# Kernel tuning notes

Measured on AMD Instinct MI355X. Metric: run time of the kernel, lower is better.

Reference implementation:

```python
import jax, jax.numpy as jnp
import numpy as np

B=4; TEXT_LEN=64; IMG=256; P=16; DIM=1024; HEADS=16; LAYERS=2; MLP=4; VOCAB=50000; TDIM=256; MAXTXT=2048
HP=IMG//P; NPATCH=HP*HP; HD=DIM//HEADS; EPS=1e-5

def _ln(x, g, b):
    m = jnp.mean(x, -1, keepdims=True)
    v = jnp.mean((x - m) ** 2, -1, keepdims=True)
    return (x - m) / jnp.sqrt(v + EPS) * g + b

def _rope_cos_sin(n, d):
    inv = 1.0 / (10000.0 ** (jnp.arange(0, d, 2, dtype=jnp.float32) / d))
    f = jnp.outer(jnp.arange(n, dtype=jnp.float32), inv)
    e = jnp.concatenate([f, f], -1)  # [n, d]
    return jnp.cos(e), jnp.sin(e)

def _rot_half(x):
    # matches torch: cat((-x[...,1::2], x[...,::2]), -1)
    return jnp.concatenate([-x[..., 1::2], x[..., ::2]], -1)

def _forward(noisy_images, text_tokens, timesteps, W_tok, pos_text, W_patch, pos_img, cls_tok,
             W_t1, b_t1, W_t2, b_t2, ln1_g, ln1_b, Wq, Wk, Wv, Wo, ln2_g, ln2_b,
             Wm1, Wm2, Wada, b_ada, fn_g, fn_b, W_final, b_final):
    Bn = noisy_images.shape[0]
    # text embed: one_hot @ W_tok.T == gather of columns of W_tok [DIM, VOCAB]
    text_emb = jnp.transpose(jnp.take(W_tok, text_tokens, axis=1), (1, 2, 0)) + pos_text[:, :TEXT_LEN]
    # image patches: [B,3,HP,P,HP,P] -> [B,HP,WP,C,P,P] -> [B,NPATCH, 3*P*P]
    patches = noisy_images.reshape(Bn, 3, HP, P, HP, P).transpose(0, 2, 4, 1, 3, 5).reshape(Bn, NPATCH, 3 * P * P)
    img_emb = patches @ W_patch.T + pos_img
    img_emb = jnp.concatenate([jnp.broadcast_to(cls_tok, (Bn, 1, DIM)), img_emb], 1)
    x = jnp.concatenate([text_emb, img_emb], 1)  # [B, N, DIM]
    N = x.shape[1]
    # sinusoidal timestep embedding (dim=256)
    half = TDIM // 2
    freqs = jnp.exp(-jnp.log(10000.0) * jnp.arange(half, dtype=jnp.float32) / half)
    args = timesteps.astype(jnp.float32)[:, None] * freqs[None]
    temb_raw = jnp.concatenate([jnp.cos(args), jnp.sin(args)], -1)
    t_emb = jax.nn.silu(temb_raw @ W_t1.T + b_t1) @ W_t2.T + b_t2  # [B, DIM]
    cos, sin = _rope_cos_sin(N, HD)
    scale = HD ** -0.5
    for l in range(LAYERS):
        mod = jax.nn.silu(t_emb) @ Wada[l].T + b_ada[l]
        sh_msa, sc_msa, g_msa, sh_mlp, sc_mlp, g_mlp = jnp.split(mod, 6, -1)
        xn = _ln(x, ln1_g[l], ln1_b[l]) * (1 + sc_msa[:, None]) + sh_msa[:, None]
        q = (xn @ Wq[l].T).reshape(Bn, N, HEADS, HD).transpose(0, 2, 1, 3)
        k = (xn @ Wk[l].T).reshape(Bn, N, HEADS, HD).transpose(0, 2, 1, 3)
        v = (xn @ Wv[l].T).reshape(Bn, N, HEADS, HD).transpose(0, 2, 1, 3)
        q = q * cos + _rot_half(q) * sin
        k = k * cos + _rot_half(k) * sin
        att = jax.nn.softmax(jnp.einsum('bhnd,bhmd->bhnm', q, k) * scale, -1)
        o = jnp.einsum('bhnm,bhmd->bhnd', att, v).transpose(0, 2, 1, 3).reshape(Bn, N, DIM)
        x = x + g_msa[:, None] * (o @ Wo[l].T)
        xn2 = _ln(x, ln2_g[l], ln2_b[l]) * (1 + sc_mlp[:, None]) + sh_mlp[:, None]
        mlp = jax.nn.gelu(xn2 @ Wm1[l].T, approximate=False) @ Wm2[l].T
        x = x + g_mlp[:, None] * mlp
    img_tok = x[:, TEXT_LEN + 1:]
    out = _ln(img_tok, fn_g, fn_b) @ W_final.T + b_final  # [B, NPATCH, 3*P*P]
    out = out.reshape(Bn, HP, HP, 3, P, P).transpose(0, 3, 1, 4, 2, 5).reshape(Bn, 3, IMG, IMG)
    return out

def setup_inputs() -> dict:
    key = jax.random.key(0)
    ks = jax.random.split(key, 24)
    def n(k, shape, s=0.02):
        return (jax.random.normal(k, shape, jnp.float32) * s).astype(jnp.float32)
    inp = {}
    inp['noisy_images'] = jax.random.normal(ks[0], (B, 3, IMG, IMG), jnp.float32)
    inp['text_tokens'] = jax.random.randint(ks[1], (B, TEXT_LEN), 0, VOCAB)
    inp['timesteps'] = jax.random.randint(ks[2], (B,), 0, 1000)
    inp['W_tok'] = n(ks[3], (DIM, VOCAB))
    inp['pos_text'] = n(ks[4], (1, MAXTXT, DIM))
    inp['W_patch'] = n(ks[5], (DIM, 3 * P * P))
    inp['pos_img'] = n(ks[6], (1, NPATCH, DIM))
    inp['cls_tok'] = n(ks[7], (1, 1, DIM))
    inp['W_t1'] = n(ks[8], (DIM, TDIM)); inp['b_t1'] = jnp.zeros((DIM,), jnp.float32)
    inp['W_t2'] = n(ks[9], (DIM, DIM)); inp['b_t2'] = jnp.zeros((DIM,), jnp.float32)
    inp['ln1_g'] = jnp.ones((LAYERS, DIM), jnp.float32); inp['ln1_b'] = jnp.zeros((LAYERS, DIM), jnp.float32)
    inp['Wq'] = n(ks[10], (LAYERS, DIM, DIM))
    inp['Wk'] = n(ks[11], (LAYERS, DIM, DIM))
    inp['Wv'] = n(ks[12], (LAYERS, DIM, DIM))
    inp['Wo'] = n(ks[13], (LAYERS, DIM, DIM))
    inp['ln2_g'] = jnp.ones((LAYERS, DIM), jnp.float32); inp['ln2_b'] = jnp.zeros((LAYERS, DIM), jnp.float32)
    inp['Wm1'] = n(ks[14], (LAYERS, MLP * DIM, DIM))
    inp['Wm2'] = n(ks[15], (LAYERS, DIM, MLP * DIM))
    inp['Wada'] = n(ks[16], (LAYERS, 6 * DIM, DIM)); inp['b_ada'] = jnp.zeros((LAYERS, 6 * DIM), jnp.float32)
    inp['fn_g'] = jnp.ones((DIM,), jnp.float32); inp['fn_b'] = jnp.zeros((DIM,), jnp.float32)
    inp['W_final'] = n(ks[17], (3 * P * P, DIM)); inp['b_final'] = jnp.zeros((3 * P * P,), jnp.float32)
    return inp

def reference(noisy_images, text_tokens, timesteps, W_tok, pos_text, W_patch, pos_img, cls_tok,
              W_t1, b_t1, W_t2, b_t2, ln1_g, ln1_b, Wq, Wk, Wv, Wo, ln2_g, ln2_b,
              Wm1, Wm2, Wada, b_ada, fn_g, fn_b, W_final, b_final):
    return _forward(noisy_images, text_tokens, timesteps, W_tok, pos_text, W_patch, pos_img, cls_tok,
                    W_t1, b_t1, W_t2, b_t2, ln1_g, ln1_b, Wq, Wk, Wv, Wo, ln2_g, ln2_b,
                    Wm1, Wm2, Wada, b_ada, fn_g, fn_b, W_final, b_final)
```

## Files before the change

### kernel.cpp

```cpp
#include <hip/hip_runtime.h>
#include <math.h>

constexpr int kBn    = 4;
constexpr int kText  = 64;
constexpr int kImg   = 256;
constexpr int kDim   = 1024;
constexpr int kHeads = 16;
constexpr int kHd    = 64;
constexpr int kNp    = 256;
constexpr int kTok   = 321;
constexpr int kVocab = 50000;
constexpr int kTdim  = 256;
constexpr int kMlp   = 4096;
constexpr int kScLd  = 328;
constexpr float kEps = 1e-5f;

typedef __attribute__((ext_vector_type(8))) short short8;
typedef __attribute__((ext_vector_type(4))) float f32x4;

__device__ __forceinline__ short f2bf(float x) {
  unsigned u = __builtin_bit_cast(unsigned, x);
  unsigned r = (u + 0x7FFFu + ((u >> 16) & 1u)) >> 16;
  return (short)r;
}

struct GemmM {
  const short* A; const short* B; float* C; const float* E;
  int M, N, K, lda, ldb, ldc;
  long sA0, sA1, sB0, sB1, sC0, sC1;
  int innerB, ldE, rowsPB;
  float alpha;
  int nSplit, splitLen;
  long partStride;
};

template<int EPI, bool PART, bool OUTBF>
__global__ __launch_bounds__(256) void gemm_mfma(GemmM p) {
  int bz = blockIdx.z;
  int split = 0;
  if (PART) { split = bz % p.nSplit; bz /= p.nSplit; }
  int b1 = bz % p.innerB, b0 = bz / p.innerB;
  const short* A = p.A + b0*p.sA0 + b1*p.sA1;
  const short* B = p.B + b0*p.sB0 + b1*p.sB1;
  long cbase = b0*p.sC0 + b1*p.sC1 + (PART ? (long)split * p.partStride : 0);
  const float* E = p.E;

  int kBeg = PART ? split * p.splitLen : 0;
  int kEnd = PART ? min(p.K, kBeg + p.splitLen) : p.K;

  __shared__ short As[64*72];
  __shared__ short Bs[64*72];

  int tid  = threadIdx.x;
  int lane = tid & 63, widx = tid >> 6;
  int quad = lane >> 4, ln = lane & 15;
  int wm = (widx >> 1) * 32, wn = (widx & 1) * 32;
  int n0 = blockIdx.x * 64, m0 = blockIdx.y * 64;

  f32x4 zero = {0.f, 0.f, 0.f, 0.f};
  f32x4 acc[2][2];
  acc[0][0] = zero; acc[0][1] = zero; acc[1][0] = zero; acc[1][1] = zero;

  short8 ra[2], rb[2];
  auto issueLoads = [&](int k0) {
#pragma unroll
    for (int r = 0; r < 2; ++r) {
      int c = tid + 256*r;
      int row = c >> 3, kc = c & 7;
      int gk = k0 + kc*8;
      {
        int gm = m0 + row;
        const short* src = A + (long)gm * p.lda + gk;
        if (gm < p.M && gk + 8 <= kEnd) {
          ra[r] = *(const short8*)src;
        } else {
          short8 t = {0,0,0,0,0,0,0,0};
          if (gm < p.M) {
#pragma unroll
            for (int j = 0; j < 8; ++j) if (gk + j < kEnd) t[j] = src[j];
          }
          ra[r] = t;
        }
      }
      {
        int gn = n0 + row;
        const short* src = B + (long)gn * p.ldb + gk;
        if (gn < p.N && gk + 8 <= kEnd) {
          rb[r] = *(const short8*)src;
        } else {
          short8 t = {0,0,0,0,0,0,0,0};
          if (gn < p.N) {
#pragma unroll
            for (int j = 0; j < 8; ++j) if (gk + j < kEnd) t[j] = src[j];
          }
          rb[r] = t;
        }
      }
    }
  };

  issueLoads(kBeg);
  for (int k0 = kBeg; k0 < kEnd; k0 += 64) {
#pragma unroll
    for (int r = 0; r < 2; ++r) {
      int c = tid + 256*r;
      int row = c >> 3, kc = c & 7;
      *(short8*)&As[row*72 + kc*8] = ra[r];
      *(short8*)&Bs[row*72 + kc*8] = rb[r];
    }
    __syncthreads();
    if (k0 + 64 < kEnd) issueLoads(k0 + 64);
#pragma unroll
    for (int ks = 0; ks < 2; ++ks) {
      short8 a0 = *(const short8*)&As[(wm +      ln)*72 + ks*32 + quad*8];
      short8 a1 = *(const short8*)&As[(wm + 16 + ln)*72 + ks*32 + quad*8];
      short8 b0 = *(const short8*)&Bs[(wn +      ln)*72 + ks*32 + quad*8];
      short8 b1 = *(const short8*)&Bs[(wn + 16 + ln)*72 + ks*32 + quad*8];
      acc[0][0] = __builtin_amdgcn_mfma_f32_16x16x32_bf16(a0, b0, acc[0][0], 0, 0, 0);
      acc[0][1] = __builtin_amdgcn_mfma_f32_16x16x32_bf16(a0, b1, acc[0][1], 0, 0, 0);
      acc[1][0] = __builtin_amdgcn_mfma_f32_16x16x32_bf16(a1, b0, acc[1][0], 0, 0, 0);
      acc[1][1] = __builtin_amdgcn_mfma_f32_16x16x32_bf16(a1, b1, acc[1][1], 0, 0, 0);
    }
    __syncthreads();
  }

#pragma unroll
  for (int mi = 0; mi < 2; ++mi)
#pragma unroll
    for (int ni = 0; ni < 2; ++ni)
#pragma unroll
      for (int reg = 0; reg < 4; ++reg) {
        int gm = m0 + wm + mi*16 + quad*4 + reg;
        int gn = n0 + wn + ni*16 + ln;
        if (gm >= p.M || gn >= p.N) continue;
        long co = cbase + (long)gm * p.ldc + gn;
        float v = acc[mi][ni][reg] * p.alpha;
        if (!PART) {
          if (EPI == 1) v += E[gn];
          else if (EPI == 3) v = 0.5f*v*(1.f + erff(v*0.70710678118654752f));
          else if (EPI == 4) v += E[(long)gm*p.ldE + gn];
          else if (EPI == 5) v = p.C[co] + E[(long)(gm / p.rowsPB)*p.ldE + gn] * v;
        }
        if (OUTBF) ((short*)p.C)[co] = f2bf(v);
        else       p.C[co] = v;
      }
}

static GemmM mkm(const short* A, const short* B, float* C,
                 int M, int N, int K, int lda, int ldb, int ldc) {
  GemmM p; p.A = A; p.B = B; p.C = C; p.E = nullptr;
  p.M = M; p.N = N; p.K = K; p.lda = lda; p.ldb = ldb; p.ldc = ldc;
  p.sA0 = p.sA1 = p.sB0 = p.sB1 = p.sC0 = p.sC1 = 0;
  p.innerB = 1; p.ldE = 0; p.rowsPB = 1; p.alpha = 1.f;
  p.nSplit = 1; p.splitLen = 0; p.partStride = 0;
  return p;
}

static void run_gemm(hipStream_t s, int epi, bool outbf, const GemmM& p, int nb) {
  dim3 g((p.N + 63)/64, (p.M + 63)/64, nb), b(256, 1, 1);
  if (outbf) {
    if (epi == 3) gemm_mfma<3,false,true><<<g,b,0,s>>>(p);
    else          gemm_mfma<0,false,true><<<g,b,0,s>>>(p);
    return;
  }
  switch (epi) {
    case 0: gemm_mfma<0,false,false><<<g,b,0,s>>>(p); break;
    case 1: gemm_mfma<1,false,false><<<g,b,0,s>>>(p); break;
    case 4: gemm_mfma<4,false,false><<<g,b,0,s>>>(p); break;
    case 5: gemm_mfma<5,false,false><<<g,b,0,s>>>(p); break;
  }
}

static void run_gemm_part(hipStream_t s, const GemmM& p, int nb) {
  dim3 g((p.N + 63)/64, (p.M + 63)/64, nb * p.nSplit), b(256, 1, 1);
  gemm_mfma<0,true,false><<<g,b,0,s>>>(p);
}

template<int EPI>
__global__ __launch_bounds__(256) void reduce_split(
    const float* __restrict__ part, long partStride, int S,
    float* __restrict__ C, const float* __restrict__ E,
    int Mv, int Nv, int ldc, long sC0, long sC1, int innerB,
    int ldE, int rowsPB, int total) {
  int idx = blockIdx.x*256 + threadIdx.x;
  if (idx >= total) return;
  int n = idx % Nv;
  int m = (idx / Nv) % Mv;
  int bz = idx / (Nv * Mv);
  int b1 = bz % innerB, b0 = bz / innerB;
  long co = b0*sC0 + b1*sC1 + (long)m*ldc + n;
  float v = 0.f;
  for (int s = 0; s < S; ++s) v += part[(long)s*partStride + co];
  if (EPI == 1) v += E[n];
  else if (EPI == 3) v = 0.5f*v*(1.f + erff(v*0.70710678118654752f));
  else if (EPI == 4) v += E[(long)m*ldE + n];
  else if (EPI == 5) v = C[co] + E[(long)(m / rowsPB)*ldE + n] * v;
  C[co] = v;
}

static void run_reduce(hipStream_t st, int epi, const float* part, long pStride, int S,
                       float* C, const float* E, int Mv, int Nv, int ldc,
                       long sC0, long sC1, int innerB, int nbTot, int ldE, int rowsPB) {
  int total = nbTot * Mv * Nv;
  dim3 g((total + 255)/256), b(256);
  switch (epi) {
    case 0: reduce_split<0><<<g,b,0,st>>>(part,pStride,S,C,E,Mv,Nv,ldc,sC0,sC1,innerB,ldE,rowsPB,total); break;
    case 1: reduce_split<1><<<g,b,0,st>>>(part,pStride,S,C,E,Mv,Nv,ldc,sC0,sC1,innerB,ldE,rowsPB,total); break;
    case 3: reduce_split<3><<<g,b,0,st>>>(part,pStride,S,C,E,Mv,Nv,ldc,sC0,sC1,innerB,ldE,rowsPB,total); break;
    case 4: reduce_split<4><<<g,b,0,st>>>(part,pStride,S,C,E,Mv,Nv,ldc,sC0,sC1,innerB,ldE,rowsPB,total); break;
    case 5: reduce_split<5><<<g,b,0,st>>>(part,pStride,S,C,E,Mv,Nv,ldc,sC0,sC1,innerB,ldE,rowsPB,total); break;
  }
}

__global__ __launch_bounds__(256) void cvt_bf16(const float* __restrict__ src,
                                                short* __restrict__ dst, int n8) {
  int i = blockIdx.x*256 + threadIdx.x;
  if (i >= n8) return;
  float4 a = ((const float4*)src)[2*i];
  float4 b = ((const float4*)src)[2*i + 1];
  short8 o;
  o[0]=f2bf(a.x); o[1]=f2bf(a.y); o[2]=f2bf(a.z); o[3]=f2bf(a.w);
  o[4]=f2bf(b.x); o[5]=f2bf(b.y); o[6]=f2bf(b.z); o[7]=f2bf(b.w);
  *(short8*)(dst + 8L*i) = o;
}

static void cvt(hipStream_t s, const float* src, short* dst, long n) {
  long n8 = n / 8;
  cvt_bf16<<<dim3((unsigned)((n8 + 255)/256)), dim3(256), 0, s>>>(src, dst, (int)n8);
}

template<int EPI>
__global__ __launch_bounds__(256) void gemv4(const float* __restrict__ A,
                                             const float* __restrict__ B,
                                             float* __restrict__ C,
                                             const float* __restrict__ bias,
                                             int N, int K, int ldc) {
  int wave = threadIdx.x >> 6, lane = threadIdx.x & 63;
  int n = blockIdx.x * 4 + wave;
  if (n >= N) return;
  const float* Brow = B + (long)n * K;
  float acc0 = 0.f, acc1 = 0.f, acc2 = 0.f, acc3 = 0.f;
  for (int k = lane * 4; k < K; k += 256) {
    float4 b = *(const float4*)(Brow + k);
    float4 a0 = *(const float4*)(A + 0*K + k);
    float4 a1 = *(const float4*)(A + 1*K + k);
    float4 a2 = *(const float4*)(A + 2*K + k);
    float4 a3 = *(const float4*)(A + 3*K + k);
    acc0 += a0.x*b.x + a0.y*b.y + a0.z*b.z + a0.w*b.w;
    acc1 += a1.x*b.x + a1.y*b.y + a1.z*b.z + a1.w*b.w;
    acc2 += a2.x*b.x + a2.y*b.y + a2.z*b.z + a2.w*b.w;
    acc3 += a3.x*b.x + a3.y*b.y + a3.z*b.z + a3.w*b.w;
  }
#pragma unroll
  for (int off = 32; off; off >>= 1) {
    acc0 += __shfl_xor(acc0, off);
    acc1 += __shfl_xor(acc1, off);
    acc2 += __shfl_xor(acc2, off);
    acc3 += __shfl_xor(acc3, off);
  }
  if (lane == 0) {
    float bs = bias[n];
    float v[4] = {acc0 + bs, acc1 + bs, acc2 + bs, acc3 + bs};
#pragma unroll
    for (int m = 0; m < 4; ++m) {
      float x = v[m];
      if (EPI == 2) x = x / (1.f + expf(-x));
      C[(long)m * ldc + n] = x;
    }
  }
}

__global__ void embed_text_cls(const float* __restrict__ Wtok, const int* __restrict__ toks,
                               const float* __restrict__ pos_text, const float* __restrict__ cls_tok,
                               float* __restrict__ x) {
  int idx = blockIdx.x*256 + threadIdx.x;
  int d = idx % kDim;
  int t = (idx / kDim) % (kText + 1);
  int b = idx / (kDim * (kText + 1));
  float v;
  if (t < kText) {
    int tok = toks[b*kText + t];
    v = Wtok[(long)d*kVocab + tok] + pos_text[(long)t*kDim + d];
  } else {
    v = cls_tok[d];
  }
  x[((long)b*kTok + t)*kDim + d] = v;
}

__global__ void extract_patches(const float* __restrict__ img, short* __restrict__ pat) {
  int idx = blockIdx.x*256 + threadIdx.x;
  int k = idx % 768;
  int p = (idx/768) % kNp;
  int b = idx/(768*kNp);
  int c = k >> 8, py = (k >> 4) & 15, px = k & 15;
  int hp = p >> 4, wp = p & 15;
  pat[idx] = f2bf(img[(((long)(b*3 + c))*kImg + hp*16 + py)*kImg + wp*16 + px]);
}

__global__ void time_freqs(const int* __restrict__ ts, float* __restrict__ temb) {
  int b = blockIdx.x, i = threadIdx.x;
  float f = expf(-9.210340371976184f * (float)i / 128.f);
  float a = (float)ts[b] * f;
  temb[b*kTdim + i] = cosf(a);
  temb[b*kTdim + 128 + i] = sinf(a);
}

__global__ void silu_kernel(const float* __restrict__ in, float* __restrict__ outp, int n) {
  int i = blockIdx.x*256 + threadIdx.x;
  if (i < n) { float x = in[i]; outp[i] = x / (1.f + expf(-x)); }
}

__device__ __forceinline__ float block_sum(float v) {
  __shared__ float sh[4];
  for (int off = 32; off; off >>= 1) v += __shfl_down(v, off);
  if ((threadIdx.x & 63) == 0) sh[threadIdx.x >> 6] = v;
  __syncthreads();
  float s = sh[0] + sh[1] + sh[2] + sh[3];
  __syncthreads();
  return s;
}

__global__ __launch_bounds__(256) void ln_mod_kernel(
    const float* __restrict__ x, const float* __restrict__ g, const float* __restrict__ be,
    const float* __restrict__ mod, int shOff, int scOff, short* __restrict__ outp) {
  int row = blockIdx.x;
  int b = row / kTok;
  const float* xr = x + (long)row*kDim;
  float s = 0.f, s2 = 0.f;
  for (int i = threadIdx.x; i < kDim; i += 256) { float v = xr[i]; s += v; s2 += v*v; }
  s = block_sum(s); s2 = block_sum(s2);
  float m = s / kDim;
  float inv = rsqrtf(s2 / kDim - m*m + kEps);
  const float* mb = mod + (long)b*(6*kDim);
  for (int i = threadIdx.x; i < kDim; i += 256) {
    float xn = (xr[i] - m)*inv*g[i] + be[i];
    outp[(long)row*kDim + i] = f2bf(xn*(1.f + mb[scOff + i]) + mb[shOff + i]);
  }
}

__global__ __launch_bounds__(256) void final_ln_kernel(
    const float* __restrict__ x, const float* __restrict__ g, const float* __restrict__ be,
    short* __restrict__ yn) {
  int row = blockIdx.x;
  int b = row / kNp, p = row % kNp;
  const float* xr = x + ((long)(b*kTok + kText + 1 + p))*kDim;
  float s = 0.f, s2 = 0.f;
  for (int i = threadIdx.x; i < kDim; i += 256) { float v = xr[i]; s += v; s2 += v*v; }
  s = block_sum(s); s2 = block_sum(s2);
  float m = s / kDim;
  float inv = rsqrtf(s2 / kDim - m*m + kEps);
  for (int i = threadIdx.x; i < kDim; i += 256)
    yn[(long)row*kDim + i] = f2bf((xr[i] - m)*inv*g[i] + be[i]);
}

__global__ __launch_bounds__(256) void rope_bf16(const float* __restrict__ qkv,
                                                 short* __restrict__ qb,
                                                 short* __restrict__ kb) {
  int idx = blockIdx.x*256 + threadIdx.x;
  int d = idx & (kDim - 1);
  int r = idx >> 10;
  int n = r % kTok;
  int hd = d & 63;
  int j = hd & 31;
  float inv = expf(-9.210340371976184f * (float)j / 32.f);
  float ang = (float)n * inv;
  float c = cosf(ang), s = sinf(ang);
  const float* row = qkv + (long)r * (3*kDim);
  int base = d - hd;
  float qv = row[d], kv = row[kDim + d];
  float qr, kr;
  if (hd < 32) { qr = -row[base + 2*hd + 1];      kr = -row[kDim + base + 2*hd + 1]; }
  else         { qr =  row[base + 2*(hd - 32)];   kr =  row[kDim + base + 2*(hd - 32)]; }
  qb[idx] = f2bf(qv*c + qr*s);
  kb[idx] = f2bf(kv*c + kr*s);
}

__global__ __launch_bounds__(256) void vtrans_kernel(const float* __restrict__ qkv,
                                                     short* __restrict__ vtb) {
  int idx = blockIdx.x*256 + threadIdx.x;
  int tok = idx % kScLd;
  int hd  = (idx / kScLd) % kHd;
  int h   = (idx / (kScLd*kHd)) % kHeads;
  int b   = idx / (kScLd*kHd*kHeads);
  float v = 0.f;
  if (tok < kTok) v = qkv[((long)(b*kTok + tok))*(3*kDim) + 2*kDim + h*kHd + hd];
  vtb[idx] = f2bf(v);
}

__global__ void softmax_rows(float* __restrict__ sc, short* __restrict__ dst,
                             int rowLen, int rowStride) {
  long row = blockIdx.x;
  float* r = sc + row*rowStride;
  short* d = dst + row*rowStride;
  int t = threadIdx.x;
  float mx = -1e30f;
  for (int i = t; i < rowLen; i += 64) mx = fmaxf(mx, r[i]);
  for (int off = 32; off; off >>= 1) mx = fmaxf(mx, __shfl_xor(mx, off));
  float sum = 0.f;
  for (int i = t; i < rowLen; i += 64) { float e = expf(r[i] - mx); r[i] = e; sum += e; }
  for (int off = 32; off; off >>= 1) sum += __shfl_xor(sum, off);
  float invs = 1.f / sum;
  for (int i = t; i < rowLen; i += 64) d[i] = f2bf(r[i] * invs);
}

__global__ void unpatchify(const float* __restrict__ op, float* __restrict__ outp) {
  int idx = blockIdx.x*256 + threadIdx.x;
  int w = idx & 255;
  int h = (idx >> 8) & 255;
  int c = (idx >> 16) % 3;
  int b = idx / (3 * kImg * kImg);
  int hp = h >> 4, py = h & 15, wp = w >> 4, px = w & 15;
  outp[idx] = op[((long)(b*kNp + hp*16 + wp))*768 + c*256 + py*16 + px];
}

extern "C" void kernel_launch(void* const* d_in, const int* in_sizes, int n_in,
                              void* d_out, int out_size, void* d_ws, size_t ws_size,
                              hipStream_t stream) {
  (void)in_sizes; (void)n_in; (void)out_size;
  const float* noisy    = (const float*)d_in[0];
  const int*   toks     = (const int*)d_in[1];
  const int*   tsteps   = (const int*)d_in[2];
  const float* W_tok    = (const float*)d_in[3];
  const float* pos_text = (const float*)d_in[4];
  const float* W_patch  = (const float*)d_in[5];
  const float* pos_img  = (const float*)d_in[6];
  const float* cls_tok  = (const float*)d_in[7];
  const float* W_t1     = (const float*)d_in[8];
  const float* b_t1     = (const float*)d_in[9];
  const float* W_t2     = (const float*)d_in[10];
  const float* b_t2     = (const float*)d_in[11];
  const float* ln1_g    = (const float*)d_in[12];
  const float* ln1_b    = (const float*)d_in[13];
  const float* Wq       = (const float*)d_in[14];
  const float* Wk       = (const float*)d_in[15];
  const float* Wv       = (const float*)d_in[16];
  const float* Wo       = (const float*)d_in[17];
  const float* ln2_g    = (const float*)d_in[18];
  const float* ln2_b    = (const float*)d_in[19];
  const float* Wm1      = (const float*)d_in[20];
  const float* Wm2      = (const float*)d_in[21];
  const float* Wada     = (const float*)d_in[22];
  const float* b_ada    = (const float*)d_in[23];
  const float* fn_g     = (const float*)d_in[24];
  const float* fn_b     = (const float*)d_in[25];
  const float* W_final  = (const float*)d_in[26];
  const float* b_final  = (const float*)d_in[27];
  float* out = (float*)d_out;

  float* ws = (float*)d_ws;
  auto alloc = [&](long nf) { float* r = ws; ws += nf; return r; };

  const long seqSz = (long)kBn * kTok * kDim;
  float* x    = alloc(seqSz);
  float* qkv  = alloc((long)kBn*kTok*3*kDim);
  float* sc   = alloc((long)kBn*kHeads*kTok*kScLd);
  short* xnb  = (short*)alloc(seqSz/2);
  short* qb   = (short*)alloc(seqSz/2);
  short* kb   = (short*)alloc(seqSz/2);
  short* ob   = (short*)alloc(seqSz/2);
  short* vtb  = (short*)alloc((long)kBn*kHeads*kHd*kScLd/2);
  short* scb  = (short*)alloc((long)kBn*kHeads*kTok*kScLd/2);
  short* patb = (short*)alloc((long)kBn*kNp*768/2);
  short* ynb  = (short*)alloc((long)kBn*kNp*kDim/2);
  short* wbuf = (short*)alloc((long)kMlp*kDim/2);
  float* temb = alloc(kBn*kTdim);
  float* t1   = alloc(kBn*kDim);
  float* temb2= alloc(kBn*kDim);
  float* st   = alloc(kBn*kDim);
  float* mod  = alloc(2L*kBn*6*kDim);
  short* hb   = (short*)sc;
  float* outp = qkv;

  const long scrStride = seqSz;
  float* scr = alloc(4*scrStride);
  bool split_ok = ((char*)ws - (char*)d_ws) <= (long)ws_size;

  embed_text_cls<<<(kBn*(kText+1)*kDim)/256, 256, 0, stream>>>(W_tok, toks, pos_text, cls_tok, x);
  extract_patches<<<(kBn*kNp*768)/256, 256, 0, stream>>>(noisy, patb);
  cvt(stream, W_patch, wbuf, (long)kDim*768);
  {
    GemmM p = mkm(patb, wbuf, split_ok ? scr : (x + (kText+1)*kDim),
                  kNp, kDim, 768, 768, 768, kDim);
    p.sA0 = (long)kNp*768; p.sC0 = (long)kTok*kDim;
    if (split_ok) {
      p.nSplit = 3; p.splitLen = 256; p.partStride = scrStride;
      run_gemm_part(stream, p, kBn);
      run_reduce(stream, 4, scr, scrStride, 3, x + (kText+1)*kDim, pos_img,
                 kNp, kDim, kDim, (long)kTok*kDim, 0, 1, kBn, kDim, 1);
    } else {
      p.E = pos_img; p.ldE = kDim;
      run_gemm(stream, 4, false, p, kBn);
    }
  }
  time_freqs<<<kBn, 128, 0, stream>>>(tsteps, temb);
  gemv4<2><<<kDim/4, 256, 0, stream>>>(temb, W_t1, t1, b_t1, kDim, kTdim, kDim);
  gemv4<1><<<kDim/4, 256, 0, stream>>>(t1, W_t2, temb2, b_t2, kDim, kDim, kDim);
  silu_kernel<<<(kBn*kDim + 255)/256, 256, 0, stream>>>(temb2, st, kBn*kDim);

  for (int l = 0; l < 2; ++l) {
    const float* Wq_l  = Wq  + (long)l*kDim*kDim;
    const float* Wk_l  = Wk  + (long)l*kDim*kDim;
    const float* Wv_l  = Wv  + (long)l*kDim*kDim;
    const float* Wo_l  = Wo  + (long)l*kDim*kDim;
    const float* Wm1_l = Wm1 + (long)l*kMlp*kDim;
    const float* Wm2_l = Wm2 + (long)l*kDim*kMlp;
    float* mod_l = mod + (long)l*kBn*6*kDim;

    gemv4<1><<<(6*kDim)/4, 256, 0, stream>>>(st, Wada + (long)l*6*kDim*kDim, mod_l,
                                             b_ada + (long)l*6*kDim, 6*kDim, kDim, 6*kDim);

    ln_mod_kernel<<<kBn*kTok, 256, 0, stream>>>(x, ln1_g + l*kDim, ln1_b + l*kDim,
                                                mod_l, 0, kDim, xnb);
    cvt(stream, Wq_l, wbuf,                   (long)kDim*kDim);
    cvt(stream, Wk_l, wbuf +   (long)kDim*kDim, (long)kDim*kDim);
    cvt(stream, Wv_l, wbuf + 2L*(long)kDim*kDim, (long)kDim*kDim);
    {
      GemmM p = mkm(xnb, wbuf, qkv, kBn*kTok, 3*kDim, kDim, kDim, kDim, 3*kDim);
      run_gemm(stream, 0, false, p, 1);
    }
    rope_bf16<<<(int)(seqSz/256), 256, 0, stream>>>(qkv, qb, kb);
    vtrans_kernel<<<(kBn*kHeads*kHd*kScLd)/256, 256, 0, stream>>>(qkv, vtb);

    {
      GemmM p = mkm(qb, kb, sc, kTok, kTok, kHd, kDim, kDim, kScLd);
      p.sA0 = (long)kTok*kDim; p.sA1 = kHd;
      p.sB0 = (long)kTok*kDim; p.sB1 = kHd;
      p.sC0 = (long)kHeads*kTok*kScLd; p.sC1 = (long)kTok*kScLd;
      p.innerB = kHeads; p.alpha = 0.125f;
      run_gemm(stream, 0, false, p, kBn*kHeads);
    }
    softmax_rows<<<kBn*kHeads*kTok, 64, 0, stream>>>(sc, scb, kTok, kScLd);
    {
      GemmM p = mkm(scb, vtb, (float*)ob, kTok, kHd, kTok, kScLd, kScLd, kDim);
      p.sA0 = (long)kHeads*kTok*kScLd; p.sA1 = (long)kTok*kScLd;
      p.sB0 = (long)kHeads*kHd*kScLd;  p.sB1 = (long)kHd*kScLd;
      p.sC0 = (long)kTok*kDim;         p.sC1 = kHd;
      p.innerB = kHeads;
      run_gemm(stream, 0, true, p, kBn*kHeads);
    }
    cvt(stream, Wo_l, wbuf, (long)kDim*kDim);
    {
      GemmM p = mkm(ob, wbuf, split_ok ? scr : x, kBn*kTok, kDim, kDim, kDim, kDim, kDim);
      if (split_ok) {
        p.nSplit = 4; p.splitLen = 256; p.partStride = scrStride;
        run_gemm_part(stream, p, 1);
        run_reduce(stream, 5, scr, scrStride, 4, x, mod_l + 2*kDim,
                   kBn*kTok, kDim, kDim, 0, 0, 1, 1, 6*kDim, kTok);
      } else {
        p.E = mod_l + 2*kDim; p.ldE = 6*kDim; p.rowsPB = kTok;
        run_gemm(stream, 5, false, p, 1);
      }
    }
    ln_mod_kernel<<<kBn*kTok, 256, 0, stream>>>(x, ln2_g + l*kDim, ln2_b + l*kDim,
                                                mod_l, 3*kDim, 4*kDim, xnb);
    cvt(stream, Wm1_l, wbuf, (long)kMlp*kDim);
    {
      GemmM p = mkm(xnb, wbuf, (float*)hb, kBn*kTok, kMlp, kDim, kDim, kDim, kMlp);
      run_gemm(stream, 3, true, p, 1);
    }
    cvt(stream, Wm2_l, wbuf, (long)kMlp*kDim);
    {
      GemmM p = mkm(hb, wbuf, split_ok ? scr : x, kBn*kTok, kDim, kMlp, kMlp, kMlp, kDim);
      if (split_ok) {
        p.nSplit = 4; p.splitLen = 1024; p.partStride = scrStride;
        run_gemm_part(stream, p, 1);
        run_reduce(stream, 5, scr, scrStride, 4, x, mod_l + 5*kDim,
                   kBn*kTok, kDim, kDim, 0, 0, 1, 1, 6*kDim, kTok);
      } else {
        p.E = mod_l + 5*kDim; p.ldE = 6*kDim; p.rowsPB = kTok;
        run_gemm(stream, 5, false, p, 1);
      }
    }
  }

  final_ln_kernel<<<kBn*kNp, 256, 0, stream>>>(x, fn_g, fn_b, ynb);
  cvt(stream, W_final, wbuf, (long)768*kDim);
  {
    GemmM p = mkm(ynb, wbuf, split_ok ? scr : outp, kBn*kNp, 768, kDim, kDim, kDim, 768);
    if (split_ok) {
      p.nSplit = 4; p.splitLen = 256; p.partStride = (long)kBn*kNp*768;
      run_gemm_part(stream, p, 1);
      run_reduce(stream, 1, scr, (long)kBn*kNp*768, 4, outp, b_final,
                 kBn*kNp, 768, 768, 0, 0, 1, 1, 0, 1);
    } else {
      p.E = b_final;
      run_gemm(stream, 1, false, p, 1);
    }
  }
  unpatchify<<<(kBn*3*kImg*kImg)/256, 256, 0, stream>>>(outp, out);
}
```

Measured before the change: 823.2 us.

## Add direct-to-LDS double-buffered GEMM, pre-convert weights, fuse reductions with LayerNorm

Adds a new GEMM kernel that loads A/B tiles straight into XOR-swizzled, double-buffered LDS with global_load_lds. It replaces the register-staged padded-LDS path for every GEMM except P·V. All bf16 weight conversions are batched into a few launches at the start, and both adaLN gemvs are hoisted ahead of the layer loop. Split-K reductions are fused into the following residual+LayerNorm kernels and into unpatchify, and softmax now processes four rows per block. The new GEMM has no M/K bounds checks, so partial tiles read rows past M, which risks out-of-range reads on non-multiple-of-64 shapes.

New measurement: 790.5 us. 1.04x faster.

```diff
diff --git a/kernel.cpp b/kernel.cpp
--- a/kernel.cpp
+++ b/kernel.cpp
@@ -24,6 +24,12 @@
   return (short)r;
 }
 
+__device__ __forceinline__ void glds16(const short* g, short* l) {
+  __builtin_amdgcn_global_load_lds(
+      (const __attribute__((address_space(1))) unsigned int*)g,
+      (__attribute__((address_space(3))) unsigned int*)l, 16, 0, 0);
+}
+
 struct GemmM {
   const short* A; const short* B; float* C; const float* E;
   int M, N, K, lda, ldb, ldc;
@@ -34,8 +40,17 @@
   long partStride;
 };
 
+__device__ __forceinline__ float epi_apply(int EPI, const GemmM& p, const float* E,
+                                           long co, int gm, int gn, float v) {
+  if (EPI == 1) v += E[gn];
+  else if (EPI == 3) v = 0.5f*v*(1.f + erff(v*0.70710678118654752f));
+  else if (EPI == 4) v += E[(long)gm*p.ldE + gn];
+  else if (EPI == 5) v = p.C[co] + E[(long)(gm / p.rowsPB)*p.ldE + gn] * v;
+  return v;
+}
+
 template<int EPI, bool PART, bool OUTBF>
-__global__ __launch_bounds__(256) void gemm_mfma(GemmM p) {
+__global__ __launch_bounds__(256) void gemm_gl(GemmM p) {
   int bz = blockIdx.z;
   int split = 0;
   if (PART) { split = bz % p.nSplit; bz /= p.nSplit; }
@@ -48,6 +63,89 @@
   int kBeg = PART ? split * p.splitLen : 0;
   int kEnd = PART ? min(p.K, kBeg + p.splitLen) : p.K;
 
+  __shared__ short As[2][64*64];
+  __shared__ short Bs[2][64*64];
+
+  int tid  = threadIdx.x;
+  int lane = tid & 63, widx = tid >> 6;
+  int quad = lane >> 4, ln = lane & 15;
+  int wm = (widx >> 1) * 32, wn = (widx & 1) * 32;
+  int n0 = blockIdx.x * 64, m0 = blockIdx.y * 64;
+
+  int l3 = lane >> 3, l7 = lane & 7;
+  int kofs = (l7 ^ l3) * 8;
+  const short* gA0 = A + (long)(m0 + 16*widx + l3) * p.lda + kofs;
+  const short* gA1 = gA0 + (long)8 * p.lda;
+  const short* gB0 = B + (long)(n0 + 16*widx + l3) * p.ldb + kofs;
+  const short* gB1 = gB0 + (long)8 * p.ldb;
+  short* lA0 = &As[0][(2*widx)*512];
+  short* lA1 = &As[0][(2*widx+1)*512];
+  short* lB0 = &Bs[0][(2*widx)*512];
+  short* lB1 = &Bs[0][(2*widx+1)*512];
+
+  auto stage = [&](int buf, int k0) {
+    int bo = buf * 4096;
+    glds16(gA0 + k0, lA0 + bo);
+    glds16(gA1 + k0, lA1 + bo);
+    glds16(gB0 + k0, lB0 + bo);
+    glds16(gB1 + k0, lB1 + bo);
+  };
+
+  f32x4 zero = {0.f, 0.f, 0.f, 0.f};
+  f32x4 acc[2][2];
+  acc[0][0] = zero; acc[0][1] = zero; acc[1][0] = zero; acc[1][1] = zero;
+
+  stage(0, kBeg);
+  int buf = 0;
+  for (int k0 = kBeg; k0 < kEnd; k0 += 64) {
+    if (k0 + 64 < kEnd) stage(buf ^ 1, k0 + 64);
+    __syncthreads();
+    const char* Ab = (const char*)&As[buf][0];
+    const char* Bb = (const char*)&Bs[buf][0];
+#pragma unroll
+    for (int ks = 0; ks < 2; ++ks) {
+      int cb = ks*64 + quad*16;
+      int r0 = wm + ln, r1 = wm + 16 + ln, r2 = wn + ln, r3 = wn + 16 + ln;
+      short8 a0 = *(const short8*)(Ab + r0*128 + (cb ^ ((r0 & 7) << 4)));
+      short8 a1 = *(const short8*)(Ab + r1*128 + (cb ^ ((r1 & 7) << 4)));
+      short8 b0 = *(const short8*)(Bb + r2*128 + (cb ^ ((r2 & 7) << 4)));
+      short8 b1 = *(const short8*)(Bb + r3*128 + (cb ^ ((r3 & 7) << 4)));
+      acc[0][0] = __builtin_amdgcn_mfma_f32_16x16x32_bf16(a0, b0, acc[0][0], 0, 0, 0);
+      acc[0][1] = __builtin_amdgcn_mfma_f32_16x16x32_bf16(a0, b1, acc[0][1], 0, 0, 0);
+      acc[1][0] = __builtin_amdgcn_mfma_f32_16x16x32_bf16(a1, b0, acc[1][0], 0, 0, 0);
+      acc[1][1] = __builtin_amdgcn_mfma_f32_16x16x32_bf16(a1, b1, acc[1][1], 0, 0, 0);
+    }
+    __syncthreads();
+    buf ^= 1;
+  }
+
+#pragma unroll
+  for (int mi = 0; mi < 2; ++mi)
+#pragma unroll
+    for (int ni = 0; ni < 2; ++ni)
+#pragma unroll
+      for (int reg = 0; reg < 4; ++reg) {
+        int gm = m0 + wm + mi*16 + quad*4 + reg;
+        int gn = n0 + wn + ni*16 + ln;
+        if (gm >= p.M || gn >= p.N) continue;
+        long co = cbase + (long)gm * p.ldc + gn;
+        float v = acc[mi][ni][reg] * p.alpha;
+        if (!PART) v = epi_apply(EPI, p, E, co, gm, gn, v);
+        if (OUTBF) ((short*)p.C)[co] = f2bf(v);
+        else       p.C[co] = v;
+      }
+}
+
+template<int EPI, bool OUTBF>
+__global__ __launch_bounds__(256) void gemm_mfma(GemmM p) {
+  int bz = blockIdx.z;
+  int b1 = bz % p.innerB, b0 = bz / p.innerB;
+  const short* A = p.A + b0*p.sA0 + b1*p.sA1;
+  const short* B = p.B + b0*p.sB0 + b1*p.sB1;
+  long cbase = b0*p.sC0 + b1*p.sC1;
+  const float* E = p.E;
+  int kEnd = p.K;
+
   __shared__ short As[64*72];
   __shared__ short Bs[64*72];
 
@@ -71,9 +169,8 @@
       {
         int gm = m0 + row;
         const short* src = A + (long)gm * p.lda + gk;
-        if (gm < p.M && gk + 8 <= kEnd) {
-          ra[r] = *(const short8*)src;
-        } else {
+        if (gm < p.M && gk + 8 <= kEnd) ra[r] = *(const short8*)src;
+        else {
           short8 t = {0,0,0,0,0,0,0,0};
           if (gm < p.M) {
 #pragma unroll
@@ -85,9 +182,8 @@
       {
         int gn = n0 + row;
         const short* src = B + (long)gn * p.ldb + gk;
-        if (gn < p.N && gk + 8 <= kEnd) {
-          rb[r] = *(const short8*)src;
-        } else {
+        if (gn < p.N && gk + 8 <= kEnd) rb[r] = *(const short8*)src;
+        else {
           short8 t = {0,0,0,0,0,0,0,0};
           if (gn < p.N) {
 #pragma unroll
@@ -99,8 +195,8 @@
     }
   };
 
-  issueLoads(kBeg);
-  for (int k0 = kBeg; k0 < kEnd; k0 += 64) {
+  issueLoads(0);
+  for (int k0 = 0; k0 < kEnd; k0 += 64) {
 #pragma unroll
     for (int r = 0; r < 2; ++r) {
       int c = tid + 256*r;
@@ -135,12 +231,7 @@
         if (gm >= p.M || gn >= p.N) continue;
         long co = cbase + (long)gm * p.ldc + gn;
         float v = acc[mi][ni][reg] * p.alpha;
-        if (!PART) {
-          if (EPI == 1) v += E[gn];
-          else if (EPI == 3) v = 0.5f*v*(1.f + erff(v*0.70710678118654752f));
-          else if (EPI == 4) v += E[(long)gm*p.ldE + gn];
-          else if (EPI == 5) v = p.C[co] + E[(long)(gm / p.rowsPB)*p.ldE + gn] * v;
-        }
+        v = epi_apply(EPI, p, E, co, gm, gn, v);
         if (OUTBF) ((short*)p.C)[co] = f2bf(v);
         else       p.C[co] = v;
       }
@@ -156,77 +247,68 @@
   return p;
 }
 
-static void run_gemm(hipStream_t s, int epi, bool outbf, const GemmM& p, int nb) {
+static void run_gl(hipStream_t s, int epi, bool outbf, const GemmM& p, int nb) {
   dim3 g((p.N + 63)/64, (p.M + 63)/64, nb), b(256, 1, 1);
   if (outbf) {
-    if (epi == 3) gemm_mfma<3,false,true><<<g,b,0,s>>>(p);
-    else          gemm_mfma<0,false,true><<<g,b,0,s>>>(p);
+    if (epi == 3) gemm_gl<3,false,true><<<g,b,0,s>>>(p);
+    else          gemm_gl<0,false,true><<<g,b,0,s>>>(p);
     return;
   }
   switch (epi) {
-    case 0: gemm_mfma<0,false,false><<<g,b,0,s>>>(p); break;
-    case 1: gemm_mfma<1,false,false><<<g,b,0,s>>>(p); break;
-    case 4: gemm_mfma<4,false,false><<<g,b,0,s>>>(p); break;
-    case 5: gemm_mfma<5,false,false><<<g,b,0,s>>>(p); break;
-  }
-}
-
-static void run_gemm_part(hipStream_t s, const GemmM& p, int nb) {
+    case 0: gemm_gl<0,false,false><<<g,b,0,s>>>(p); break;
+    case 1: gemm_gl<1,false,false><<<g,b,0,s>>>(p); break;
+    case 4: gemm_gl<4,false,false><<<g,b,0,s>>>(p); break;
+    case 5: gemm_gl<5,false,false><<<g,b,0,s>>>(p); break;
+  }
+}
+
+static void run_gl_part(hipStream_t s, const GemmM& p, int nb) {
   dim3 g((p.N + 63)/64, (p.M + 63)/64, nb * p.nSplit), b(256, 1, 1);
-  gemm_mfma<0,true,false><<<g,b,0,s>>>(p);
-}
-
-template<int EPI>
-__global__ __launch_bounds__(256) void reduce_split(
+  gemm_gl<0,true,false><<<g,b,0,s>>>(p);
+}
+
+static void run_pv(hipStream_t s, const GemmM& p, int nb) {
+  dim3 g((p.N + 63)/64, (p.M + 63)/64, nb), b(256, 1, 1);
+  gemm_mfma<0,true><<<g,b,0,s>>>(p);
+}
+
+__global__ __launch_bounds__(256) void reduce_epi4(
     const float* __restrict__ part, long partStride, int S,
     float* __restrict__ C, const float* __restrict__ E,
-    int Mv, int Nv, int ldc, long sC0, long sC1, int innerB,
-    int ldE, int rowsPB, int total) {
+    int Mv, int Nv, int ldc, long sC0, int ldE, int total) {
   int idx = blockIdx.x*256 + threadIdx.x;
   if (idx >= total) return;
   int n = idx % Nv;
   int m = (idx / Nv) % Mv;
-  int bz = idx / (Nv * Mv);
-  int b1 = bz % innerB, b0 = bz / innerB;
-  long co = b0*sC0 + b1*sC1 + (long)m*ldc + n;
+  int b0 = idx / (Nv * Mv);
+  long co = b0*sC0 + (long)m*ldc + n;
   float v = 0.f;
   for (int s = 0; s < S; ++s) v += part[(long)s*partStride + co];
-  if (EPI == 1) v += E[n];
-  else if (EPI == 3) v = 0.5f*v*(1.f + erff(v*0.70710678118654752f));
-  else if (EPI == 4) v += E[(long)m*ldE + n];
-  else if (EPI == 5) v = C[co] + E[(long)(m / rowsPB)*ldE + n] * v;
+  v += E[(long)m*ldE + n];
   C[co] = v;
 }
 
-static void run_reduce(hipStream_t st, int epi, const float* part, long pStride, int S,
-                       float* C, const float* E, int Mv, int Nv, int ldc,
-                       long sC0, long sC1, int innerB, int nbTot, int ldE, int rowsPB) {
-  int total = nbTot * Mv * Nv;
-  dim3 g((total + 255)/256), b(256);
-  switch (epi) {
-    case 0: reduce_split<0><<<g,b,0,st>>>(part,pStride,S,C,E,Mv,Nv,ldc,sC0,sC1,innerB,ldE,rowsPB,total); break;
-    case 1: reduce_split<1><<<g,b,0,st>>>(part,pStride,S,C,E,Mv,Nv,ldc,sC0,sC1,innerB,ldE,rowsPB,total); break;
-    case 3: reduce_split<3><<<g,b,0,st>>>(part,pStride,S,C,E,Mv,Nv,ldc,sC0,sC1,innerB,ldE,rowsPB,total); break;
-    case 4: reduce_split<4><<<g,b,0,st>>>(part,pStride,S,C,E,Mv,Nv,ldc,sC0,sC1,innerB,ldE,rowsPB,total); break;
-    case 5: reduce_split<5><<<g,b,0,st>>>(part,pStride,S,C,E,Mv,Nv,ldc,sC0,sC1,innerB,ldE,rowsPB,total); break;
-  }
-}
-
-__global__ __launch_bounds__(256) void cvt_bf16(const float* __restrict__ src,
-                                                short* __restrict__ dst, int n8) {
+__global__ __launch_bounds__(256) void cvt2_bf16(const float* __restrict__ src,
+                                                 short* __restrict__ dst, int n8,
+                                                 long srcStride, long dstStride, int total8) {
   int i = blockIdx.x*256 + threadIdx.x;
-  if (i >= n8) return;
-  float4 a = ((const float4*)src)[2*i];
-  float4 b = ((const float4*)src)[2*i + 1];
+  if (i >= total8) return;
+  int l = i / n8, j = i % n8;
+  const float* s = src + srcStride*l + (long)8*j;
+  short* d = dst + dstStride*l + (long)8*j;
+  float4 a = *(const float4*)s;
+  float4 b = *(const float4*)(s + 4);
   short8 o;
   o[0]=f2bf(a.x); o[1]=f2bf(a.y); o[2]=f2bf(a.z); o[3]=f2bf(a.w);
   o[4]=f2bf(b.x); o[5]=f2bf(b.y); o[6]=f2bf(b.z); o[7]=f2bf(b.w);
-  *(short8*)(dst + 8L*i) = o;
-}
-
-static void cvt(hipStream_t s, const float* src, short* dst, long n) {
-  long n8 = n / 8;
-  cvt_bf16<<<dim3((unsigned)((n8 + 255)/256)), dim3(256), 0, s>>>(src, dst, (int)n8);
+  *(short8*)d = o;
+}
+
+static void cvtT(hipStream_t s, const float* src, short* dst, long nPerLayer,
+                 long srcStride, long dstStride, int L) {
+  int n8 = (int)(nPerLayer / 8);
+  int total8 = n8 * L;
+  cvt2_bf16<<<dim3((total8 + 255)/256), dim3(256), 0, s>>>(src, dst, n8, srcStride, dstStride, total8);
 }
 
 template<int EPI>
@@ -338,6 +420,38 @@
   }
 }
 
+__global__ __launch_bounds__(256) void ln_mod_red_kernel(
+    const float* __restrict__ xin, const float* __restrict__ part, long pStride, int S,
+    const float* __restrict__ gate, const float* __restrict__ g, const float* __restrict__ be,
+    const float* __restrict__ mod, int shOff, int scOff,
+    float* __restrict__ xout, short* __restrict__ outp) {
+  int row = blockIdx.x;
+  int b = row / kTok;
+  long base = (long)row*kDim;
+  const float* gt = gate + (long)b*(6*kDim);
+  float v[4];
+  float s = 0.f, s2 = 0.f;
+#pragma unroll
+  for (int c = 0; c < 4; ++c) {
+    int i = threadIdx.x + 256*c;
+    float acc = 0.f;
+    for (int sp = 0; sp < S; ++sp) acc += part[(long)sp*pStride + base + i];
+    float xv = xin[base + i] + gt[i] * acc;
+    v[c] = xv; s += xv; s2 += xv*xv;
+  }
+  s = block_sum(s); s2 = block_sum(s2);
+  float m = s / kDim;
+  float inv = rsqrtf(s2 / kDim - m*m + kEps);
+  const float* mb = mod + (long)b*(6*kDim);
+#pragma unroll
+  for (int c = 0; c < 4; ++c) {
+    int i = threadIdx.x + 256*c;
+    xout[base + i] = v[c];
+    float xn = (v[c] - m)*inv*g[i] + be[i];
+    outp[base + i] = f2bf(xn*(1.f + mb[scOff + i]) + mb[shOff + i]);
+  }
+}
+
 __global__ __launch_bounds__(256) void final_ln_kernel(
     const float* __restrict__ x, const float* __restrict__ g, const float* __restrict__ be,
     short* __restrict__ yn) {
@@ -351,6 +465,34 @@
   float inv = rsqrtf(s2 / kDim - m*m + kEps);
   for (int i = threadIdx.x; i < kDim; i += 256)
     yn[(long)row*kDim + i] = f2bf((xr[i] - m)*inv*g[i] + be[i]);
+}
+
+__global__ __launch_bounds__(256) void final_ln_red_kernel(
+    const float* __restrict__ xin, const float* __restrict__ part, long pStride, int S,
+    const float* __restrict__ gate, const float* __restrict__ g, const float* __restrict__ be,
+    short* __restrict__ yn) {
+  int row = blockIdx.x;
+  int b = row / kNp, p = row % kNp;
+  long xb = ((long)(b*kTok + kText + 1 + p))*kDim;
+  const float* gt = gate + (long)b*(6*kDim);
+  float v[4];
+  float s = 0.f, s2 = 0.f;
+#pragma unroll
+  for (int c = 0; c < 4; ++c) {
+    int i = threadIdx.x + 256*c;
+    float acc = 0.f;
+    for (int sp = 0; sp < S; ++sp) acc += part[(long)sp*pStride + xb + i];
+    float xv = xin[xb + i] + gt[i] * acc;
+    v[c] = xv; s += xv; s2 += xv*xv;
+  }
+  s = block_sum(s); s2 = block_sum(s2);
+  float m = s / kDim;
+  float inv = rsqrtf(s2 / kDim - m*m + kEps);
+#pragma unroll
+  for (int c = 0; c < 4; ++c) {
+    int i = threadIdx.x + 256*c;
+    yn[(long)row*kDim + i] = f2bf((v[c] - m)*inv*g[i] + be[i]);
+  }
 }
 
 __global__ __launch_bounds__(256) void rope_bf16(const float* __restrict__ qkv,
@@ -387,20 +529,21 @@
   vtb[idx] = f2bf(v);
 }
 
-__global__ void softmax_rows(float* __restrict__ sc, short* __restrict__ dst,
-                             int rowLen, int rowStride) {
-  long row = blockIdx.x;
-  float* r = sc + row*rowStride;
-  short* d = dst + row*rowStride;
-  int t = threadIdx.x;
+__global__ __launch_bounds__(256) void softmax_rows4(float* __restrict__ sc,
+                                                     short* __restrict__ dst, int nRows) {
+  int wid = threadIdx.x >> 6, t = threadIdx.x & 63;
+  int row = blockIdx.x*4 + wid;
+  if (row >= nRows) return;
+  float* r = sc + (long)row*kScLd;
+  short* d = dst + (long)row*kScLd;
   float mx = -1e30f;
-  for (int i = t; i < rowLen; i += 64) mx = fmaxf(mx, r[i]);
+  for (int i = t; i < kTok; i += 64) mx = fmaxf(mx, r[i]);
   for (int off = 32; off; off >>= 1) mx = fmaxf(mx, __shfl_xor(mx, off));
   float sum = 0.f;
-  for (int i = t; i < rowLen; i += 64) { float e = expf(r[i] - mx); r[i] = e; sum += e; }
+  for (int i = t; i < kTok; i += 64) { float e = expf(r[i] - mx); r[i] = e; sum += e; }
   for (int off = 32; off; off >>= 1) sum += __shfl_xor(sum, off);
   float invs = 1.f / sum;
-  for (int i = t; i < rowLen; i += 64) d[i] = f2bf(r[i] * invs);
+  for (int i = t; i < kTok; i += 64) d[i] = f2bf(r[i] * invs);
 }
 
 __global__ void unpatchify(const float* __restrict__ op, float* __restrict__ outp) {
@@ -411,6 +554,20 @@
   int b = idx / (3 * kImg * kImg);
   int hp = h >> 4, py = h & 15, wp = w >> 4, px = w & 15;
   outp[idx] = op[((long)(b*kNp + hp*16 + wp))*768 + c*256 + py*16 + px];
+}
+
+__global__ void unpatchify_red(const float* __restrict__ part, long pStride, int S,
+                               const float* __restrict__ bias, float* __restrict__ outp) {
+  int idx = blockIdx.x*256 + threadIdx.x;
+  int w = idx & 255;
+  int h = (idx >> 8) & 255;
+  int c = (idx >> 16) % 3;
+  int b = idx / (3 * kImg * kImg);
+  int hp = h >> 4, py = h & 15, wp = w >> 4, px = w & 15;
+  long co = ((long)(b*kNp + hp*16 + wp))*768 + c*256 + py*16 + px;
+  float v = bias[c*256 + py*16 + px];
+  for (int s = 0; s < S; ++s) v += part[(long)s*pStride + co];
+  outp[idx] = v;
 }
 
 extern "C" void kernel_launch(void* const* d_in, const int* in_sizes, int n_in,
@@ -462,7 +619,6 @@
   short* scb  = (short*)alloc((long)kBn*kHeads*kTok*kScLd/2);
   short* patb = (short*)alloc((long)kBn*kNp*768/2);
   short* ynb  = (short*)alloc((long)kBn*kNp*kDim/2);
-  short* wbuf = (short*)alloc((long)kMlp*kDim/2);
   float* temb = alloc(kBn*kTdim);
   float* t1   = alloc(kBn*kDim);
   float* temb2= alloc(kBn*kDim);
@@ -471,52 +627,66 @@
   short* hb   = (short*)sc;
   float* outp = qkv;
 
+  const long oPatch = 0;
+  const long nPatch = (long)kDim*768;
+  const long perLayer = 3L*kDim*kDim + (long)kDim*kDim + 2L*kMlp*kDim;
+  const long oLayer = nPatch;
+  const long oFinal = nPatch + 2*perLayer;
+  const long nFinal = (long)768*kDim;
+  short* wAr = (short*)alloc((nPatch + 2*perLayer + nFinal)/2);
+
   const long scrStride = seqSz;
   float* scr = alloc(4*scrStride);
   bool split_ok = ((char*)ws - (char*)d_ws) <= (long)ws_size;
 
+  cvtT(stream, W_patch, wAr + oPatch, nPatch, 0, 0, 1);
+  cvtT(stream, Wq,  wAr + oLayer + 0,               (long)kDim*kDim, (long)kDim*kDim, perLayer, 2);
+  cvtT(stream, Wk,  wAr + oLayer + (long)kDim*kDim, (long)kDim*kDim, (long)kDim*kDim, perLayer, 2);
+  cvtT(stream, Wv,  wAr + oLayer + 2L*kDim*kDim,    (long)kDim*kDim, (long)kDim*kDim, perLayer, 2);
+  cvtT(stream, Wo,  wAr + oLayer + 3L*kDim*kDim,    (long)kDim*kDim, (long)kDim*kDim, perLayer, 2);
+  cvtT(stream, Wm1, wAr + oLayer + 4L*kDim*kDim,    (long)kMlp*kDim, (long)kMlp*kDim, perLayer, 2);
+  cvtT(stream, Wm2, wAr + oLayer + 4L*kDim*kDim + (long)kMlp*kDim,
+       (long)kMlp*kDim, (long)kMlp*kDim, perLayer, 2);
+  cvtT(stream, W_final, wAr + oFinal, nFinal, 0, 0, 1);
+
   embed_text_cls<<<(kBn*(kText+1)*kDim)/256, 256, 0, stream>>>(W_tok, toks, pos_text, cls_tok, x);
   extract_patches<<<(kBn*kNp*768)/256, 256, 0, stream>>>(noisy, patb);
-  cvt(stream, W_patch, wbuf, (long)kDim*768);
   {
-    GemmM p = mkm(patb, wbuf, split_ok ? scr : (x + (kText+1)*kDim),
+    GemmM p = mkm(patb, wAr + oPatch, split_ok ? scr : (x + (kText+1)*kDim),
                   kNp, kDim, 768, 768, 768, kDim);
     p.sA0 = (long)kNp*768; p.sC0 = (long)kTok*kDim;
     if (split_ok) {
       p.nSplit = 3; p.splitLen = 256; p.partStride = scrStride;
-      run_gemm_part(stream, p, kBn);
-      run_reduce(stream, 4, scr, scrStride, 3, x + (kText+1)*kDim, pos_img,
-                 kNp, kDim, kDim, (long)kTok*kDim, 0, 1, kBn, kDim, 1);
+      run_gl_part(stream, p, kBn);
+      int total = kBn*kNp*kDim;
+      reduce_epi4<<<(total+255)/256, 256, 0, stream>>>(scr, scrStride, 3,
+          x + (kText+1)*kDim, pos_img, kNp, kDim, kDim, (long)kTok*kDim, kDim, total);
     } else {
       p.E = pos_img; p.ldE = kDim;
-      run_gemm(stream, 4, false, p, kBn);
+      run_gl(stream, 4, false, p, kBn);
     }
   }
   time_freqs<<<kBn, 128, 0, stream>>>(tsteps, temb);
   gemv4<2><<<kDim/4, 256, 0, stream>>>(temb, W_t1, t1, b_t1, kDim, kTdim, kDim);
   gemv4<1><<<kDim/4, 256, 0, stream>>>(t1, W_t2, temb2, b_t2, kDim, kDim, kDim);
   silu_kernel<<<(kBn*kDim + 255)/256, 256, 0, stream>>>(temb2, st, kBn*kDim);
+  for (int l = 0; l < 2; ++l)
+    gemv4<1><<<(6*kDim)/4, 256, 0, stream>>>(st, Wada + (long)l*6*kDim*kDim,
+                                             mod + (long)l*kBn*6*kDim,
+                                             b_ada + (long)l*6*kDim, 6*kDim, kDim, 6*kDim);
+
+  ln_mod_kernel<<<kBn*kTok, 256, 0, stream>>>(x, ln1_g, ln1_b, mod, 0, kDim, xnb);
 
   for (int l = 0; l < 2; ++l) {
-    const float* Wq_l  = Wq  + (long)l*kDim*kDim;
-    const float* Wk_l  = Wk  + (long)l*kDim*kDim;
-    const float* Wv_l  = Wv  + (long)l*kDim*kDim;
-    const float* Wo_l  = Wo  + (long)l*kDim*kDim;
-    const float* Wm1_l = Wm1 + (long)l*kMlp*kDim;
-    const float* Wm2_l = Wm2 + (long)l*kDim*kMlp;
+    const short* wqkv_l = wAr + oLayer + (long)l*perLayer;
+    const short* wo_l   = wqkv_l + 3L*kDim*kDim;
+    const short* wm1_l  = wqkv_l + 4L*kDim*kDim;
+    const short* wm2_l  = wm1_l + (long)kMlp*kDim;
     float* mod_l = mod + (long)l*kBn*6*kDim;
 
-    gemv4<1><<<(6*kDim)/4, 256, 0, stream>>>(st, Wada + (long)l*6*kDim*kDim, mod_l,
-                                             b_ada + (long)l*6*kDim, 6*kDim, kDim, 6*kDim);
-
-    ln_mod_kernel<<<kBn*kTok, 256, 0, stream>>>(x, ln1_g + l*kDim, ln1_b + l*kDim,
-                                                mod_l, 0, kDim, xnb);
-    cvt(stream, Wq_l, wbuf,                   (long)kDim*kDim);
-    cvt(stream, Wk_l, wbuf +   (long)kDim*kDim, (long)kDim*kDim);
-    cvt(stream, Wv_l, wbuf + 2L*(long)kDim*kDim, (long)kDim*kDim);
     {
-      GemmM p = mkm(xnb, wbuf, qkv, kBn*kTok, 3*kDim, kDim, kDim, kDim, 3*kDim);
-      run_gemm(stream, 0, false, p, 1);
+      GemmM p = mkm(xnb, wqkv_l, qkv, kBn*kTok, 3*kDim, kDim, kDim, kDim, 3*kDim);
+      run_gl(stream, 0, false, p, 1);
     }
     rope_bf16<<<(int)(seqSz/256), 256, 0, stream>>>(qkv, qb, kb);
     vtrans_kernel<<<(kBn*kHeads*kHd*kScLd)/256, 256, 0, stream>>>(qkv, vtb);
@@ -527,65 +697,74 @@
       p.sB0 = (long)kTok*kDim; p.sB1 = kHd;
       p.sC0 = (long)kHeads*kTok*kScLd; p.sC1 = (long)kTok*kScLd;
       p.innerB = kHeads; p.alpha = 0.125f;
-      run_gemm(stream, 0, false, p, kBn*kHeads);
-    }
-    softmax_rows<<<kBn*kHeads*kTok, 64, 0, stream>>>(sc, scb, kTok, kScLd);
+      run_gl(stream, 0, false, p, kBn*kHeads);
+    }
+    {
+      int nRows = kBn*kHeads*kTok;
+      softmax_rows4<<<(nRows+3)/4, 256, 0, stream>>>(sc, scb, nRows);
+    }
     {
       GemmM p = mkm(scb, vtb, (float*)ob, kTok, kHd, kTok, kScLd, kScLd, kDim);
       p.sA0 = (long)kHeads*kTok*kScLd; p.sA1 = (long)kTok*kScLd;
       p.sB0 = (long)kHeads*kHd*kScLd;  p.sB1 = (long)kHd*kScLd;
       p.sC0 = (long)kTok*kDim;         p.sC1 = kHd;
       p.innerB = kHeads;
-      run_gemm(stream, 0, true, p, kBn*kHeads);
-    }
-    cvt(stream, Wo_l, wbuf, (long)kDim*kDim);
+      run_pv(stream, p, kBn*kHeads);
+    }
     {
-      GemmM p = mkm(ob, wbuf, split_ok ? scr : x, kBn*kTok, kDim, kDim, kDim, kDim, kDim);
+      GemmM p = mkm(ob, wo_l, split_ok ? scr : x, kBn*kTok, kDim, kDim, kDim, kDim, kDim);
       if (split_ok) {
         p.nSplit = 4; p.splitLen = 256; p.partStride = scrStride;
-        run_gemm_part(stream, p, 1);
-        run_reduce(stream, 5, scr, scrStride, 4, x, mod_l + 2*kDim,
-                   kBn*kTok, kDim, kDim, 0, 0, 1, 1, 6*kDim, kTok);
+        run_gl_part(stream, p, 1);
+        ln_mod_red_kernel<<<kBn*kTok, 256, 0, stream>>>(x, scr, scrStride, 4,
+            mod_l + 2*kDim, ln2_g + l*kDim, ln2_b + l*kDim, mod_l, 3*kDim, 4*kDim, x, xnb);
       } else {
         p.E = mod_l + 2*kDim; p.ldE = 6*kDim; p.rowsPB = kTok;
-        run_gemm(stream, 5, false, p, 1);
+        run_gl(stream, 5, false, p, 1);
+        ln_mod_kernel<<<kBn*kTok, 256, 0, stream>>>(x, ln2_g + l*kDim, ln2_b + l*kDim,
+                                                    mod_l, 3*kDim, 4*kDim, xnb);
       }
     }
-    ln_mod_kernel<<<kBn*kTok, 256, 0, stream>>>(x, ln2_g + l*kDim, ln2_b + l*kDim,
-                                                mod_l, 3*kDim, 4*kDim, xnb);
-    cvt(stream, Wm1_l, wbuf, (long)kMlp*kDim);
     {
-      GemmM p = mkm(xnb, wbuf, (float*)hb, kBn*kTok, kMlp, kDim, kDim, kDim, kMlp);
-      run_gemm(stream, 3, true, p, 1);
-    }
-    cvt(stream, Wm2_l, wbuf, (long)kMlp*kDim);
+      GemmM p = mkm(xnb, wm1_l, (float*)hb, kBn*kTok, kMlp, kDim, kDim, kDim, kMlp);
+      run_gl(stream, 3, true, p, 1);
+    }
     {
-      GemmM p = mkm(hb, wbuf, split_ok ? scr : x, kBn*kTok, kDim, kMlp, kMlp, kMlp, kDim);
+      GemmM p = mkm(hb, wm2_l, split_ok ? scr : x, kBn*kTok, kDim, kMlp, kMlp, kMlp, kDim);
       if (split_ok) {
         p.nSplit = 4; p.splitLen = 1024; p.partStride = scrStride;
-        run_gemm_part(stream, p, 1);
-        run_reduce(stream, 5, scr, scrStride, 4, x, mod_l + 5*kDim,
-                   kBn*kTok, kDim, kDim, 0, 0, 1, 1, 6*kDim, kTok);
+        run_gl_part(stream, p, 1);
+        if (l == 0) {
+          ln_mod_red_kernel<<<kBn*kTok, 256, 0, stream>>>(x, scr, scrStride, 4,
+              mod_l + 5*kDim, ln1_g + kDim, ln1_b + kDim,
+              mod + (long)kBn*6*kDim, 0, kDim, x, xnb);
+        } else {
+          final_ln_red_kernel<<<kBn*kNp, 256, 0, stream>>>(x, scr, scrStride, 4,
+              mod_l + 5*kDim, fn_g, fn_b, ynb);
+        }
       } else {
         p.E = mod_l + 5*kDim; p.ldE = 6*kDim; p.rowsPB = kTok;
-        run_gemm(stream, 5, false, p, 1);
+        run_gl(stream, 5, false, p, 1);
+        if (l == 0)
+          ln_mod_kernel<<<kBn*kTok, 256, 0, stream>>>(x, ln1_g + kDim, ln1_b + kDim,
+                                                      mod + (long)kBn*6*kDim, 0, kDim, xnb);
+        else
+          final_ln_kernel<<<kBn*kNp, 256, 0, stream>>>(x, fn_g, fn_b, ynb);
       }
     }
   }
 
-  final_ln_kernel<<<kBn*kNp, 256, 0, stream>>>(x, fn_g, fn_b, ynb);
-  cvt(stream, W_final, wbuf, (long)768*kDim);
   {
-    GemmM p = mkm(ynb, wbuf, split_ok ? scr : outp, kBn*kNp, 768, kDim, kDim, kDim, 768);
+    GemmM p = mkm(ynb, wAr + oFinal, split_ok ? scr : outp, kBn*kNp, 768, kDim, kDim, kDim, 768);
     if (split_ok) {
       p.nSplit = 4; p.splitLen = 256; p.partStride = (long)kBn*kNp*768;
-      run_gemm_part(stream, p, 1);
-      run_reduce(stream, 1, scr, (long)kBn*kNp*768, 4, outp, b_final,
-                 kBn*kNp, 768, 768, 0, 0, 1, 1, 0, 1);
+      run_gl_part(stream, p, 1);
+      unpatchify_red<<<(kBn*3*kImg*kImg)/256, 256, 0, stream>>>(scr, (long)kBn*kNp*768, 4,
+                                                                b_final, out);
     } else {
       p.E = b_final;
-      run_gemm(stream, 1, false, p, 1);
-    }
-  }
-  unpatchify<<<(kBn*3*kImg*kImg)/256, 256, 0, stream>>>(outp, out);
-}
+      run_gl(stream, 1, false, p, 1);
+      unpatchify<<<(kBn*3*kImg*kImg)/256, 256, 0, stream>>>(outp, out);
+    }
+  }
+}
```
